# Kernel optimization log

Measured on AMD Instinct MI355X. Metric: run time of the kernel, lower is better.

Reference implementation:

```python
import jax, jax.numpy as jnp
import numpy as np

EMB = 2048
HEADS = 16
HEAD_DIM = EMB // HEADS
LATENT = 512
B, S = 2, 2048


def setup_inputs() -> dict:
    key = jax.random.key(0)
    ks = jax.random.split(key, 7)
    sc = lambda fan_in: 1.0 / np.sqrt(fan_in)
    return {
        "x": jax.random.normal(ks[0], (B, S, EMB), dtype=jnp.float32),
        "w_q": jax.random.normal(ks[1], (EMB, EMB), dtype=jnp.float32) * sc(EMB),
        "w_down": jax.random.normal(ks[2], (LATENT, EMB), dtype=jnp.float32) * sc(EMB),
        "w_up_k": jax.random.normal(ks[3], (EMB, LATENT), dtype=jnp.float32) * sc(LATENT),
        "w_up_v": jax.random.normal(ks[4], (EMB, LATENT), dtype=jnp.float32) * sc(LATENT),
        "w_out": jax.random.normal(ks[5], (EMB, EMB), dtype=jnp.float32) * sc(EMB),
        "b_out": jax.random.normal(ks[6], (EMB,), dtype=jnp.float32) * 0.01,
    }


def reference(x, w_q, w_down, w_up_k, w_up_v, w_out, b_out):
    # Linear uses torch convention: y = x @ W.T
    q = jnp.einsum("bse,fe->bsf", x, w_q)          # [B,S,EMB]
    latent = jnp.einsum("bse,le->bsl", x, w_down)  # [B,S,LATENT]
    k = jnp.einsum("bsl,fl->bsf", latent, w_up_k)
    v = jnp.einsum("bsl,fl->bsf", latent, w_up_v)

    def heads(t):  # [B,S,EMB] -> [B,H,S,D]
        return t.reshape(B, S, HEADS, HEAD_DIM).transpose(0, 2, 1, 3)

    qh, kh, vh = heads(q), heads(k), heads(v)
    scores = jnp.einsum("bhqd,bhkd->bhqk", qh, kh)  # [B,H,S,S]
    qpos = jnp.arange(S)
    causal = qpos[:, None] < qpos[None, :]          # True where future (masked)
    scores = jnp.where(causal[None, None], -jnp.inf, scores)
    attn = jax.nn.softmax(scores / np.sqrt(HEAD_DIM).astype(np.float32), axis=-1)
    ctx = jnp.einsum("bhqk,bhkd->bhqd", attn, vh)   # [B,H,S,D]
    ctx = ctx.transpose(0, 2, 1, 3).reshape(B, S, EMB)
    return jnp.einsum("bse,fe->bsf", ctx, w_out) + b_out
```

## Files before the change

kernel.cpp:

```cpp
#include <hip/hip_runtime.h>
#include <hip/hip_bf16.h>

#define EMB 2048
#define HEADS 16
#define HDIM 128
#define LATENT 512
#define BATCH 2
#define SEQ 2048
#define MROWS (BATCH*SEQ)

typedef __attribute__((ext_vector_type(4))) float f32x4;
typedef __attribute__((ext_vector_type(8))) short s16x8;

__device__ __forceinline__ unsigned short f2bf(float f) {
  __hip_bfloat16 h = __float2bfloat16(f);
  union { __hip_bfloat16 h; unsigned short u; } c; c.h = h; return c.u;
}

#define GLOAD_LDS16(g, l) \
  __builtin_amdgcn_global_load_lds((const __attribute__((address_space(1))) unsigned int*)(g), \
                                   (__attribute__((address_space(3))) unsigned int*)(l), 16, 0, 0)

__global__ void cvt_kernel(const float* __restrict__ src, unsigned short* __restrict__ dst, int n4) {
  int i = blockIdx.x * blockDim.x + threadIdx.x;
  int stride = gridDim.x * blockDim.x;
  for (; i < n4; i += stride) {
    float4 v = reinterpret_cast<const float4*>(src)[i];
    ushort4 o;
    o.x = f2bf(v.x); o.y = f2bf(v.y); o.z = f2bf(v.z); o.w = f2bf(v.w);
    reinterpret_cast<ushort4*>(dst)[i] = o;
  }
}

#define BM 128
#define BN 128
#define BK 32

template<int OUTF32>
__global__ __launch_bounds__(256) void gemm_bt(
    const unsigned short* __restrict__ A, const unsigned short* __restrict__ B,
    void* __restrict__ C, const float* __restrict__ bias, int M, int N, int K)
{
  __shared__ __align__(16) unsigned short sA[BM][BK];
  __shared__ __align__(16) unsigned short sB[BN][BK];
  const int tid  = threadIdx.x;
  const int lane = tid & 63, wave = tid >> 6;
  const int wm = wave >> 1, wn = wave & 1;
  const int lrow = lane & 15, kgrp = lane >> 4;

  const int gx = gridDim.x;
  const int nwg = gx * gridDim.y;
  const int orig = blockIdx.y * gx + blockIdx.x;
  const int chunk = nwg >> 3;
  const int sw = (orig & 7) * chunk + (orig >> 3);
  const long bm = (long)(sw / gx) * BM, bn = (long)(sw % gx) * BN;

  const int srow = tid >> 2;
  const int scol = (tid & 3) * 8;

  f32x4 zero4 = {0.f, 0.f, 0.f, 0.f};
  f32x4 acc[4][4];
  #pragma unroll
  for (int i = 0; i < 4; ++i)
    #pragma unroll
    for (int j = 0; j < 4; ++j) acc[i][j] = zero4;

  const unsigned short* ga = A + (bm + srow) * (long)K + scol;
  const unsigned short* gb = B + (bn + srow) * (long)K + scol;

  for (int k0 = 0; k0 < K; k0 += BK) {
    GLOAD_LDS16(ga + k0,                 &sA[srow][scol]);
    GLOAD_LDS16(ga + 64*(long)K + k0,    &sA[srow + 64][scol]);
    GLOAD_LDS16(gb + k0,                 &sB[srow][scol]);
    GLOAD_LDS16(gb + 64*(long)K + k0,    &sB[srow + 64][scol]);
    __syncthreads();

    s16x8 aF[4], bF[4];
    #pragma unroll
    for (int i = 0; i < 4; ++i) {
      aF[i] = *reinterpret_cast<const s16x8*>(&sA[wm*64 + i*16 + lrow][kgrp*8]);
      bF[i] = *reinterpret_cast<const s16x8*>(&sB[wn*64 + i*16 + lrow][kgrp*8]);
    }
    #pragma unroll
    for (int i = 0; i < 4; ++i)
      #pragma unroll
      for (int j = 0; j < 4; ++j)
        acc[i][j] = __builtin_amdgcn_mfma_f32_16x16x32_bf16(aF[i], bF[j], acc[i][j], 0, 0, 0);
    __syncthreads();
  }

  #pragma unroll
  for (int i = 0; i < 4; ++i) {
    #pragma unroll
    for (int j = 0; j < 4; ++j) {
      long row = bm + wm*64 + i*16 + kgrp*4;
      long col = bn + wn*64 + j*16 + lrow;
      if (OUTF32) {
        float* Cf = (float*)C;
        float bv = bias[col];
        #pragma unroll
        for (int r = 0; r < 4; ++r) Cf[(row + r) * (long)N + col] = acc[i][j][r] + bv;
      } else {
        unsigned short* Cb = (unsigned short*)C;
        #pragma unroll
        for (int r = 0; r < 4; ++r) Cb[(row + r) * (long)N + col] = f2bf(acc[i][j][r]);
      }
    }
  }
}

#define KVB 64
#define QTB 64
#define NQT3 (SEQ/QTB)

__global__ __launch_bounds__(256, 2) void attn3_kernel(
    const unsigned short* __restrict__ Q, const unsigned short* __restrict__ Kg,
    const unsigned short* __restrict__ Vt, unsigned short* __restrict__ CTX)
{
  const int pr = blockIdx.x, h = blockIdx.y, b = blockIdx.z;
  const int tid = threadIdx.x, w = tid >> 6, lane = tid & 63;
  const int lrow = lane & 15, kgrp = lane >> 4;
  const size_t bS = (size_t)b * SEQ;

  __shared__ __align__(16) unsigned short sK[2][KVB * HDIM];
  __shared__ __align__(16) unsigned short sP[4][16][72];

  const int krow  = tid >> 4;
  const int kcolB = ((tid & 15) * 16) ^ (((tid >> 4) & 7) << 4);
  const unsigned short* kst_g = Kg + (bS + krow) * EMB + h * HDIM + (kcolB >> 1);

  const int swz = (lrow & 7) << 4;
  int cc[4];
  #pragma unroll
  for (int kk = 0; kk < 4; ++kk) cc[kk] = ((kk * 64 + kgrp * 16) ^ swz) >> 1;

  const float C = 0.12751742f;
  const float THR = 11.5f;
  f32x4 zero4 = {0.f, 0.f, 0.f, 0.f};

  const int qts[2] = {NQT3 - 1 - pr, pr};
  for (int ps = 0; ps < 2; ++ps) {
    const int qt = qts[ps];
    const int nt = qt + 1;
    const int qw = qt * QTB + w * 16;

    s16x8 qF[4];
    #pragma unroll
    for (int kk = 0; kk < 4; ++kk)
      qF[kk] = *reinterpret_cast<const s16x8*>(
          Q + (bS + qw + lrow) * EMB + h * HDIM + kk * 32 + kgrp * 8);

    f32x4 o[8];
    #pragma unroll
    for (int dt = 0; dt < 8; ++dt) o[dt] = zero4;
    float rm[4], rl[4];
    #pragma unroll
    for (int r = 0; r < 4; ++r) { rm[r] = -1.0e30f; rl[r] = 0.f; }

    __syncthreads();
    {
      unsigned short* l0 = &sK[0][0] + tid * 8;
      #pragma unroll
      for (int R = 0; R < 4; ++R) GLOAD_LDS16(kst_g + (size_t)R * 16 * EMB, l0 + R * 2048);
    }

    for (int j = 0; j < nt; ++j) {
      __syncthreads();
      const int kv0 = j * KVB;
      if (j + 1 < nt) {
        const unsigned short* gs = kst_g + (size_t)(j + 1) * KVB * EMB;
        unsigned short* ls = &sK[(j + 1) & 1][0] + tid * 8;
        #pragma unroll
        for (int R = 0; R < 4; ++R) GLOAD_LDS16(gs + (size_t)R * 16 * EMB, ls + R * 2048);
      }

      s16x8 vF[2][8];
      #pragma unroll
      for (int hf = 0; hf < 2; ++hf)
        #pragma unroll
        for (int dt = 0; dt < 8; ++dt)
          vF[hf][dt] = *reinterpret_cast<const s16x8*>(
              Vt + (size_t)(h * HDIM + dt * 16 + lrow) * MROWS + bS + kv0 + hf * 32 + kgrp * 8);

      const unsigned short* kb = &sK[j & 1][0];
      f32x4 sc[4];
      #pragma unroll
      for (int kvg = 0; kvg < 4; ++kvg) sc[kvg] = zero4;
      __builtin_amdgcn_s_setprio(1);
      #pragma unroll
      for (int kvg = 0; kvg < 4; ++kvg) {
        const int rb = (kvg * 16 + lrow) * HDIM;
        #pragma unroll
        for (int kk = 0; kk < 4; ++kk) {
          s16x8 kF = *reinterpret_cast<const s16x8*>(kb + rb + cc[kk]);
          sc[kvg] = __builtin_amdgcn_mfma_f32_16x16x32_bf16(qF[kk], kF, sc[kvg], 0, 0, 0);
        }
      }
      __builtin_amdgcn_s_setprio(0);

      const bool needm = (kv0 + 63 > qw);
      float sv[4][4];
      #pragma unroll
      for (int kvg = 0; kvg < 4; ++kvg)
        #pragma unroll
        for (int r = 0; r < 4; ++r) {
          float s = sc[kvg][r];
          if (needm) {
            int qq  = qw + kgrp * 4 + r;
            int col = kv0 + kvg * 16 + lrow;
            s = (col <= qq) ? s : -3.0e38f;
          }
          sv[kvg][r] = s;
        }
      float tm[4];
      #pragma unroll
      for (int r = 0; r < 4; ++r)
        tm[r] = fmaxf(fmaxf(sv[0][r], sv[1][r]), fmaxf(sv[2][r], sv[3][r]));
      #pragma unroll
      for (int m = 1; m < 16; m <<= 1)
        #pragma unroll
        for (int r = 0; r < 4; ++r) tm[r] = fmaxf(tm[r], __shfl_xor(tm[r], m));

      float d = tm[0] * C - rm[0];
      #pragma unroll
      for (int r = 1; r < 4; ++r) d = fmaxf(d, tm[r] * C - rm[r]);
      const bool skip = __all(d <= THR);

      float mn[4];
      #pragma unroll
      for (int r = 0; r < 4; ++r) mn[r] = skip ? rm[r] : fmaxf(rm[r], tm[r] * C);

      float ts[4];
      #pragma unroll
      for (int r = 0; r < 4; ++r) {
        float p0 = exp2f(fmaf(sv[0][r], C, -mn[r]));
        float p1 = exp2f(fmaf(sv[1][r], C, -mn[r]));
        float p2 = exp2f(fmaf(sv[2][r], C, -mn[r]));
        float p3 = exp2f(fmaf(sv[3][r], C, -mn[r]));
        ts[r] = (p0 + p1) + (p2 + p3);
        const int qrow = kgrp * 4 + r;
        sP[w][qrow][ 0 + lrow] = f2bf(p0);
        sP[w][qrow][16 + lrow] = f2bf(p1);
        sP[w][qrow][32 + lrow] = f2bf(p2);
        sP[w][qrow][48 + lrow] = f2bf(p3);
      }
      #pragma unroll
      for (int m = 1; m < 16; m <<= 1)
        #pragma unroll
        for (int r = 0; r < 4; ++r) ts[r] += __shfl_xor(ts[r], m);

      if (skip) {
        #pragma unroll
        for (int r = 0; r < 4; ++r) rl[r] += ts[r];
      } else {
        float corr[4];
        #pragma unroll
        for (int r = 0; r < 4; ++r) {
          corr[r] = exp2f(rm[r] - mn[r]);
          rm[r] = mn[r];
          rl[r] = rl[r] * corr[r] + ts[r];
        }
        #pragma unroll
        for (int dt = 0; dt < 8; ++dt)
          #pragma unroll
          for (int r = 0; r < 4; ++r) o[dt][r] *= corr[r];
      }

      s16x8 pF[2];
      #pragma unroll
      for (int hf = 0; hf < 2; ++hf)
        pF[hf] = *reinterpret_cast<const s16x8*>(&sP[w][lrow][hf * 32 + kgrp * 8]);
      __builtin_amdgcn_s_setprio(1);
      #pragma unroll
      for (int dt = 0; dt < 8; ++dt) {
        o[dt] = __builtin_amdgcn_mfma_f32_16x16x32_bf16(pF[0], vF[0][dt], o[dt], 0, 0, 0);
        o[dt] = __builtin_amdgcn_mfma_f32_16x16x32_bf16(pF[1], vF[1][dt], o[dt], 0, 0, 0);
      }
      __builtin_amdgcn_s_setprio(0);
    }

    float iv[4];
    #pragma unroll
    for (int r = 0; r < 4; ++r) iv[r] = 1.0f / rl[r];
    #pragma unroll
    for (int dt = 0; dt < 8; ++dt)
      #pragma unroll
      for (int r = 0; r < 4; ++r)
        CTX[(bS + qw + kgrp * 4 + r) * EMB + h * HDIM + dt * 16 + lrow] =
            f2bf(o[dt][r] * iv[r]);
  }
}

extern "C" void kernel_launch(void* const* d_in, const int* in_sizes, int n_in,
                              void* d_out, int out_size, void* d_ws, size_t ws_size,
                              hipStream_t stream)
{
  const float* x      = (const float*)d_in[0];
  const float* w_q    = (const float*)d_in[1];
  const float* w_down = (const float*)d_in[2];
  const float* w_upk  = (const float*)d_in[3];
  const float* w_upv  = (const float*)d_in[4];
  const float* w_out  = (const float*)d_in[5];
  const float* b_out  = (const float*)d_in[6];
  float* out = (float*)d_out;

  char* ws = (char*)d_ws;
  size_t off = 0;
  auto alloc = [&](size_t elems) {
    void* p = ws + off; off += elems * 2; off = (off + 255) & ~(size_t)255; return p;
  };
  unsigned short* xb   = (unsigned short*)alloc((size_t)MROWS * EMB);
  unsigned short* wqb  = (unsigned short*)alloc((size_t)EMB * EMB);
  unsigned short* wdb  = (unsigned short*)alloc((size_t)LATENT * EMB);
  unsigned short* wkb  = (unsigned short*)alloc((size_t)EMB * LATENT);
  unsigned short* wvb  = (unsigned short*)alloc((size_t)EMB * LATENT);
  unsigned short* wob  = (unsigned short*)alloc((size_t)EMB * EMB);
  unsigned short* qb   = (unsigned short*)alloc((size_t)MROWS * EMB);
  unsigned short* latb = (unsigned short*)alloc((size_t)MROWS * LATENT);
  unsigned short* kb   = (unsigned short*)alloc((size_t)MROWS * EMB);
  unsigned short* vtb  = (unsigned short*)alloc((size_t)EMB * MROWS);
  unsigned short* ctxb = xb;

  auto cvt = [&](const float* s, unsigned short* d, size_t n) {
    int n4 = (int)(n / 4);
    int blocks = (n4 + 255) / 256; if (blocks > 1024) blocks = 1024;
    cvt_kernel<<<dim3(blocks), dim3(256), 0, stream>>>(s, d, n4);
  };
  cvt(x,      xb,  (size_t)MROWS * EMB);
  cvt(w_q,    wqb, (size_t)EMB * EMB);
  cvt(w_down, wdb, (size_t)LATENT * EMB);
  cvt(w_upk,  wkb, (size_t)EMB * LATENT);
  cvt(w_upv,  wvb, (size_t)EMB * LATENT);
  cvt(w_out,  wob, (size_t)EMB * EMB);

  gemm_bt<0><<<dim3(EMB/BN,    MROWS/BM), 256, 0, stream>>>(xb,   wqb, qb,   nullptr, MROWS, EMB,    EMB);
  gemm_bt<0><<<dim3(LATENT/BN, MROWS/BM), 256, 0, stream>>>(xb,   wdb, latb, nullptr, MROWS, LATENT, EMB);
  gemm_bt<0><<<dim3(EMB/BN,    MROWS/BM), 256, 0, stream>>>(latb, wkb, kb,   nullptr, MROWS, EMB,    LATENT);
  gemm_bt<0><<<dim3(MROWS/BN,  EMB/BM),   256, 0, stream>>>(wvb,  latb, vtb, nullptr, EMB,   MROWS,  LATENT);

  attn3_kernel<<<dim3(NQT3/2, HEADS, BATCH), 256, 0, stream>>>(qb, kb, vtb, ctxb);

  gemm_bt<1><<<dim3(EMB/BN, MROWS/BM), 256, 0, stream>>>(ctxb, wob, (void*)out, b_out, MROWS, EMB, EMB);
}
```

Measured before the change: 454.9 us.

## Add 256x128 GEMM kernel, remap attention blocks, compute row sums via MFMA

Adds a new 512-thread GEMM with 256x128 tiles, double-buffered LDS through global_load_lds, and an XCD-aware block swizzle. It replaces the Q, K, V and output projections with it to get more operand reuse per tile. The attention kernel now uses a flattened grid remapped so neighbouring blocks share heads, and it computes softmax row sums with an MFMA against a ones vector instead of shuffle reductions. The new GEMM uses 96KB of dynamic LDS at one block per CU, so occupancy drops, and there is one-time attribute setup on the host.

```diff
diff --git a/kernel.cpp b/kernel.cpp
--- a/kernel.cpp
+++ b/kernel.cpp
@@ -109,15 +109,116 @@
   }
 }
 
+#define G2_LDS (96*1024)
+
+template<int OUTF32>
+__global__ __launch_bounds__(512, 1) void gemm256(
+    const unsigned short* __restrict__ A, const unsigned short* __restrict__ B,
+    void* __restrict__ C, const float* __restrict__ bias, int M, int N, int K)
+{
+  extern __shared__ char smem[];
+  const int tid  = threadIdx.x;
+  const int lane = tid & 63, wave = tid >> 6;
+  const int wm = wave >> 1, wn = wave & 1;
+  const int lrow = lane & 15, kgrp = lane >> 4;
+
+  const int gx = gridDim.x;
+  const int nwg = gx * gridDim.y;
+  const int orig = blockIdx.y * gx + blockIdx.x;
+  const int chunk = nwg >> 3;
+  const int sw = (orig & 7) * chunk + (orig >> 3);
+  const long bm = (long)(sw / gx) * 256, bn = (long)(sw % gx) * 128;
+
+  const int strow = tid >> 3;
+  const int scolB = ((tid & 7) * 16) ^ ((strow & 7) << 4);
+  const unsigned short* gaS = A + (bm + strow) * (long)K + (scolB >> 1);
+  const unsigned short* gbS = B + (bn + strow) * (long)K + (scolB >> 1);
+
+  int fcol[2];
+  #pragma unroll
+  for (int kh = 0; kh < 2; ++kh) fcol[kh] = (kh * 64 + kgrp * 16) ^ ((lrow & 7) << 4);
+
+  f32x4 zero4 = {0.f, 0.f, 0.f, 0.f};
+  f32x4 acc[4][4];
+  #pragma unroll
+  for (int i = 0; i < 4; ++i)
+    #pragma unroll
+    for (int j = 0; j < 4; ++j) acc[i][j] = zero4;
+
+  const int NT = K >> 6;
+  auto stage = [&](int cur, int t) {
+    const long k0 = (long)t * 64;
+    unsigned short* sa = (unsigned short*)(smem) + cur * 16384 + tid * 8;
+    unsigned short* sb = (unsigned short*)(smem + 65536) + cur * 8192 + tid * 8;
+    #pragma unroll
+    for (int R = 0; R < 4; ++R) GLOAD_LDS16(gaS + (R * 64) * (long)K + k0, sa + R * 4096);
+    #pragma unroll
+    for (int R = 0; R < 2; ++R) GLOAD_LDS16(gbS + (R * 64) * (long)K + k0, sb + R * 4096);
+  };
+
+  stage(0, 0);
+  __syncthreads();
+
+  int cur = 0;
+  for (int t = 0; t < NT; ++t) {
+    if (t + 1 < NT) stage(cur ^ 1, t + 1);
+    const char* sa = smem + cur * 32768;
+    const char* sb = smem + 65536 + cur * 16384;
+    #pragma unroll
+    for (int kh = 0; kh < 2; ++kh) {
+      s16x8 aF[4], bF[4];
+      #pragma unroll
+      for (int i = 0; i < 4; ++i)
+        aF[i] = *reinterpret_cast<const s16x8*>(sa + (wm*64 + i*16 + lrow) * 128 + fcol[kh]);
+      #pragma unroll
+      for (int j = 0; j < 4; ++j)
+        bF[j] = *reinterpret_cast<const s16x8*>(sb + (wn*64 + j*16 + lrow) * 128 + fcol[kh]);
+      __builtin_amdgcn_s_setprio(1);
+      #pragma unroll
+      for (int i = 0; i < 4; ++i)
+        #pragma unroll
+        for (int j = 0; j < 4; ++j)
+          acc[i][j] = __builtin_amdgcn_mfma_f32_16x16x32_bf16(aF[i], bF[j], acc[i][j], 0, 0, 0);
+      __builtin_amdgcn_s_setprio(0);
+    }
+    __syncthreads();
+    cur ^= 1;
+  }
+
+  #pragma unroll
+  for (int i = 0; i < 4; ++i) {
+    #pragma unroll
+    for (int j = 0; j < 4; ++j) {
+      long row = bm + wm*64 + i*16 + kgrp*4;
+      long col = bn + wn*64 + j*16 + lrow;
+      if (OUTF32) {
+        float* Cf = (float*)C;
+        float bv = bias[col];
+        #pragma unroll
+        for (int r = 0; r < 4; ++r) Cf[(row + r) * (long)N + col] = acc[i][j][r] + bv;
+      } else {
+        unsigned short* Cb = (unsigned short*)C;
+        #pragma unroll
+        for (int r = 0; r < 4; ++r) Cb[(row + r) * (long)N + col] = f2bf(acc[i][j][r]);
+      }
+    }
+  }
+}
+
 #define KVB 64
 #define QTB 64
 #define NQT3 (SEQ/QTB)
 
-__global__ __launch_bounds__(256, 2) void attn3_kernel(
+__global__ __launch_bounds__(256, 2) void attn4_kernel(
     const unsigned short* __restrict__ Q, const unsigned short* __restrict__ Kg,
     const unsigned short* __restrict__ Vt, unsigned short* __restrict__ CTX)
 {
-  const int pr = blockIdx.x, h = blockIdx.y, b = blockIdx.z;
+  const int bid = blockIdx.x;
+  const int rest = bid >> 3;
+  const int pr = rest & 15;
+  const int g = (bid & 7) + 8 * (rest >> 4);
+  const int h = g & 15, b = g >> 4;
+
   const int tid = threadIdx.x, w = tid >> 6, lane = tid & 63;
   const int lrow = lane & 15, kgrp = lane >> 4;
   const size_t bS = (size_t)b * SEQ;
@@ -137,6 +238,9 @@
   const float C = 0.12751742f;
   const float THR = 11.5f;
   f32x4 zero4 = {0.f, 0.f, 0.f, 0.f};
+  s16x8 onesF;
+  #pragma unroll
+  for (int i = 0; i < 8; ++i) onesF[i] = (short)0x3F80;
 
   const int qts[2] = {NQT3 - 1 - pr, pr};
   for (int ps = 0; ps < 2; ++ps) {
@@ -230,53 +334,45 @@
       #pragma unroll
       for (int r = 0; r < 4; ++r) mn[r] = skip ? rm[r] : fmaxf(rm[r], tm[r] * C);
 
-      float ts[4];
       #pragma unroll
       for (int r = 0; r < 4; ++r) {
         float p0 = exp2f(fmaf(sv[0][r], C, -mn[r]));
         float p1 = exp2f(fmaf(sv[1][r], C, -mn[r]));
         float p2 = exp2f(fmaf(sv[2][r], C, -mn[r]));
         float p3 = exp2f(fmaf(sv[3][r], C, -mn[r]));
-        ts[r] = (p0 + p1) + (p2 + p3);
         const int qrow = kgrp * 4 + r;
         sP[w][qrow][ 0 + lrow] = f2bf(p0);
         sP[w][qrow][16 + lrow] = f2bf(p1);
         sP[w][qrow][32 + lrow] = f2bf(p2);
         sP[w][qrow][48 + lrow] = f2bf(p3);
       }
-      #pragma unroll
-      for (int m = 1; m < 16; m <<= 1)
-        #pragma unroll
-        for (int r = 0; r < 4; ++r) ts[r] += __shfl_xor(ts[r], m);
-
-      if (skip) {
-        #pragma unroll
-        for (int r = 0; r < 4; ++r) rl[r] += ts[r];
-      } else {
-        float corr[4];
+      if (!skip) {
         #pragma unroll
         for (int r = 0; r < 4; ++r) {
-          corr[r] = exp2f(rm[r] - mn[r]);
+          float corr = exp2f(rm[r] - mn[r]);
           rm[r] = mn[r];
-          rl[r] = rl[r] * corr[r] + ts[r];
+          rl[r] *= corr;
+          #pragma unroll
+          for (int dt = 0; dt < 8; ++dt) o[dt][r] *= corr;
         }
-        #pragma unroll
-        for (int dt = 0; dt < 8; ++dt)
-          #pragma unroll
-          for (int r = 0; r < 4; ++r) o[dt][r] *= corr[r];
       }
 
       s16x8 pF[2];
       #pragma unroll
       for (int hf = 0; hf < 2; ++hf)
         pF[hf] = *reinterpret_cast<const s16x8*>(&sP[w][lrow][hf * 32 + kgrp * 8]);
+      f32x4 psum = zero4;
       __builtin_amdgcn_s_setprio(1);
+      psum = __builtin_amdgcn_mfma_f32_16x16x32_bf16(pF[0], onesF, psum, 0, 0, 0);
+      psum = __builtin_amdgcn_mfma_f32_16x16x32_bf16(pF[1], onesF, psum, 0, 0, 0);
       #pragma unroll
       for (int dt = 0; dt < 8; ++dt) {
         o[dt] = __builtin_amdgcn_mfma_f32_16x16x32_bf16(pF[0], vF[0][dt], o[dt], 0, 0, 0);
         o[dt] = __builtin_amdgcn_mfma_f32_16x16x32_bf16(pF[1], vF[1][dt], o[dt], 0, 0, 0);
       }
       __builtin_amdgcn_s_setprio(0);
+      #pragma unroll
+      for (int r = 0; r < 4; ++r) rl[r] += psum[r];
     }
 
     float iv[4];
@@ -303,6 +399,13 @@
   const float* w_out  = (const float*)d_in[5];
   const float* b_out  = (const float*)d_in[6];
   float* out = (float*)d_out;
+
+  static bool attr_done = false;
+  if (!attr_done) {
+    hipFuncSetAttribute((const void*)gemm256<0>, hipFuncAttributeMaxDynamicSharedMemorySize, G2_LDS);
+    hipFuncSetAttribute((const void*)gemm256<1>, hipFuncAttributeMaxDynamicSharedMemorySize, G2_LDS);
+    attr_done = true;
+  }
 
   char* ws = (char*)d_ws;
   size_t off = 0;
@@ -333,12 +436,12 @@
   cvt(w_upv,  wvb, (size_t)EMB * LATENT);
   cvt(w_out,  wob, (size_t)EMB * EMB);
 
-  gemm_bt<0><<<dim3(EMB/BN,    MROWS/BM), 256, 0, stream>>>(xb,   wqb, qb,   nullptr, MROWS, EMB,    EMB);
-  gemm_bt<0><<<dim3(LATENT/BN, MROWS/BM), 256, 0, stream>>>(xb,   wdb, latb, nullptr, MROWS, LATENT, EMB);
-  gemm_bt<0><<<dim3(EMB/BN,    MROWS/BM), 256, 0, stream>>>(latb, wkb, kb,   nullptr, MROWS, EMB,    LATENT);
-  gemm_bt<0><<<dim3(MROWS/BN,  EMB/BM),   256, 0, stream>>>(wvb,  latb, vtb, nullptr, EMB,   MROWS,  LATENT);
-
-  attn3_kernel<<<dim3(NQT3/2, HEADS, BATCH), 256, 0, stream>>>(qb, kb, vtb, ctxb);
-
-  gemm_bt<1><<<dim3(EMB/BN, MROWS/BM), 256, 0, stream>>>(ctxb, wob, (void*)out, b_out, MROWS, EMB, EMB);
-}
+  gemm256<0><<<dim3(EMB/128, MROWS/256), 512, G2_LDS, stream>>>(xb, wqb, qb, nullptr, MROWS, EMB, EMB);
+  gemm_bt<0><<<dim3(LATENT/BN, MROWS/BM), 256, 0, stream>>>(xb, wdb, latb, nullptr, MROWS, LATENT, EMB);
+  gemm256<0><<<dim3(EMB/128, MROWS/256), 512, G2_LDS, stream>>>(latb, wkb, kb, nullptr, MROWS, EMB, LATENT);
+  gemm256<0><<<dim3(MROWS/128, EMB/256), 512, G2_LDS, stream>>>(wvb, latb, vtb, nullptr, EMB, MROWS, LATENT);
+
+  attn4_kernel<<<dim3(512, 1, 1), 256, 0, stream>>>(qb, kb, vtb, ctxb);
+
+  gemm256<1><<<dim3(EMB/128, MROWS/256), 512, G2_LDS, stream>>>(ctxb, wob, (void*)out, b_out, MROWS, EMB, EMB);
+}
```

New measurement: 411.1 us. 9.6% less time.
